# Performance work log

Hardware: AMD Instinct MI355X
Metric: run time of the kernel (lower is better)

## Reference

```python
import jax, jax.numpy as jnp
import numpy as np

N_EMBD = 768
N_HEAD = 12
HEAD_SIZE = N_EMBD // N_HEAD  # 64
WINDOW = 64  # sliding_window_size
EPS = 1e-6


def _rmsnorm(x, g):
    xf = x.astype(jnp.float32)
    n = xf * jax.lax.rsqrt(jnp.mean(xf * xf, axis=-1, keepdims=True) + EPS)
    return n.astype(x.dtype) * g


def _gelu_tanh(x):
    c = jnp.sqrt(jnp.asarray(2.0 / jnp.pi, x.dtype))
    return 0.5 * x * (1.0 + jnp.tanh(c * (x + 0.044715 * x ** 3)))


def setup_inputs() -> dict:
    key = jax.random.key(0)
    ks = jax.random.split(key, 12)
    B, T = 8, 1024
    s = 0.02
    return {
        "x": jax.random.normal(ks[0], (B, T, N_EMBD), jnp.float32),
        "w_q": jax.random.normal(ks[1], (N_EMBD, N_HEAD, HEAD_SIZE), jnp.float32) * s,
        "w_k": jax.random.normal(ks[2], (N_EMBD, N_HEAD, HEAD_SIZE), jnp.float32) * s,
        "w_v": jax.random.normal(ks[3], (N_EMBD, N_HEAD, HEAD_SIZE), jnp.float32) * s,
        "w_proj": jax.random.normal(ks[4], (N_EMBD, N_EMBD), jnp.float32) * s,
        "b_proj": jnp.zeros((N_EMBD,), jnp.float32),
        "w_ff1": jax.random.normal(ks[5], (N_EMBD, 4 * N_EMBD), jnp.float32) * s,
        "b_ff1": jnp.zeros((4 * N_EMBD,), jnp.float32),
        "w_ff2": jax.random.normal(ks[6], (4 * N_EMBD, N_EMBD), jnp.float32) * s,
        "b_ff2": jnp.zeros((N_EMBD,), jnp.float32),
        "g1": jnp.ones((N_EMBD,), jnp.float32),
        "g2": jnp.ones((N_EMBD,), jnp.float32),
    }


def reference(x, w_q, w_k, w_v, w_proj, b_proj, w_ff1, b_ff1, w_ff2, b_ff2, g1, g2):
    B, T, C = x.shape
    # ---- multi-head sliding-window causal attention (eval: dropout = identity) ----
    h = _rmsnorm(x, g1)
    q = jnp.einsum("btc,chd->bhtd", h, w_q)
    k = jnp.einsum("btc,chd->bhtd", h, w_k)
    v = jnp.einsum("btc,chd->bhtd", h, w_v)
    scores = jnp.einsum("bhtd,bhsd->bhts", q, k) / jnp.sqrt(jnp.asarray(HEAD_SIZE, x.dtype))
    pos = jnp.arange(T)
    diff = pos[:, None] - pos[None, :]  # q_pos - k_pos
    mask = (diff < 0) | (diff >= WINDOW)  # causal + sliding window of 64
    scores = jnp.where(mask[None, None], jnp.asarray(-jnp.inf, scores.dtype), scores)
    attn = jax.nn.softmax(scores, axis=-1)
    out = jnp.einsum("bhts,bhsd->bhtd", attn, v)
    out = out.transpose(0, 2, 1, 3).reshape(B, T, C)  # concat heads
    x = x + out @ w_proj + b_proj
    # ---- feedforward ----
    h2 = _rmsnorm(x, g2)
    ff = _gelu_tanh(h2 @ w_ff1 + b_ff1) @ w_ff2 + b_ff2
    x = x + ff
    aux = jnp.asarray(0.0, jnp.float32)
    return (x, aux)
```

## Files before the change

kernel.cpp:

```cpp
#include <hip/hip_runtime.h>
#include <cstdint>

#define DEVI __device__ __forceinline__

typedef __bf16 bf16x8 __attribute__((ext_vector_type(8)));
typedef float  f32x4  __attribute__((ext_vector_type(4)));

template<int V> struct IC { static constexpr int v = V; };

DEVI unsigned short f2b(float f){
  unsigned u = __builtin_bit_cast(unsigned, f);
  unsigned r = u + 0x7FFF + ((u >> 16) & 1);
  return (unsigned short)(r >> 16);
}
DEVI float b2f(unsigned short s){
  unsigned u = ((unsigned)s) << 16;
  return __builtin_bit_cast(float, u);
}
DEVI float gelu_f(float x){
  float u = 0.7978845608028654f * (x + 0.044715f * x * x * x);
  float e = __expf(2.0f * u);
  return x * (1.0f - 1.0f / (e + 1.0f));
}
DEVI void gl_lds16(const unsigned short* g, unsigned short* l){
  __builtin_amdgcn_global_load_lds(
      (const __attribute__((address_space(1))) unsigned int*)g,
      (__attribute__((address_space(3))) unsigned int*)l, 16, 0, 0);
}

__global__ __launch_bounds__(256)
void transpose_all(const float* __restrict__ w_q, const float* __restrict__ w_k,
                   const float* __restrict__ w_v, const float* __restrict__ w_proj,
                   const float* __restrict__ w_ff1, const float* __restrict__ w_ff2,
                   unsigned short* __restrict__ WqkvT, unsigned short* __restrict__ WprojT,
                   unsigned short* __restrict__ Wff1T, unsigned short* __restrict__ Wff2T)
{
  __shared__ float tile[32][33];
  int blk = blockIdx.x;
  const float* in; unsigned short* out; int R, C, b0;
  if      (blk < 576) { in = w_q;    out = WqkvT;              R = 768;  C = 768;  b0 = 0;    }
  else if (blk < 1152){ in = w_k;    out = WqkvT + 768 * 768;  R = 768;  C = 768;  b0 = 576;  }
  else if (blk < 1728){ in = w_v;    out = WqkvT + 1536 * 768; R = 768;  C = 768;  b0 = 1152; }
  else if (blk < 2304){ in = w_proj; out = WprojT;             R = 768;  C = 768;  b0 = 1728; }
  else if (blk < 4608){ in = w_ff1;  out = Wff1T;              R = 768;  C = 3072; b0 = 2304; }
  else                { in = w_ff2;  out = Wff2T;              R = 3072; C = 768;  b0 = 4608; }
  int lb = blk - b0;
  int nbx = C >> 5;
  int bx = lb % nbx, by = lb / nbx;
  int c0 = bx << 5, r0 = by << 5;
  int tx = threadIdx.x & 31, ty = threadIdx.x >> 5;
  #pragma unroll
  for (int j = 0; j < 32; j += 8)
    tile[ty + j][tx] = in[(size_t)(r0 + ty + j) * C + c0 + tx];
  __syncthreads();
  #pragma unroll
  for (int j = 0; j < 32; j += 8)
    out[(size_t)(c0 + ty + j) * R + r0 + tx] = f2b(tile[tx][ty + j]);
}

template<bool INF32>
__global__ __launch_bounds__(256)
void rmsnorm_k(const void* __restrict__ xin, const float* __restrict__ g,
               unsigned short* __restrict__ out)
{
  int wid = threadIdx.x >> 6, lane = threadIdx.x & 63;
  size_t row = (size_t)blockIdx.x * 4 + wid;
  float v[12];
  float ss = 0.0f;
  if (INF32){
    const float* xr = (const float*)xin + row * 768;
    #pragma unroll
    for (int c = 0; c < 3; c++){
      float4 t = *(const float4*)&xr[lane * 4 + c * 256];
      v[c * 4 + 0] = t.x; v[c * 4 + 1] = t.y; v[c * 4 + 2] = t.z; v[c * 4 + 3] = t.w;
    }
  } else {
    const unsigned short* xr = (const unsigned short*)xin + row * 768;
    #pragma unroll
    for (int c = 0; c < 3; c++){
      ushort4 t = *(const ushort4*)&xr[lane * 4 + c * 256];
      v[c * 4 + 0] = b2f(t.x); v[c * 4 + 1] = b2f(t.y);
      v[c * 4 + 2] = b2f(t.z); v[c * 4 + 3] = b2f(t.w);
    }
  }
  #pragma unroll
  for (int j = 0; j < 12; j++) ss += v[j] * v[j];
  #pragma unroll
  for (int o = 32; o >= 1; o >>= 1) ss += __shfl_xor(ss, o);
  float rs = rsqrtf(ss * (1.0f / 768.0f) + 1e-6f);
  #pragma unroll
  for (int c = 0; c < 3; c++){
    const float4 gv = *(const float4*)&g[lane * 4 + c * 256];
    ushort4 o4;
    o4.x = f2b(v[c * 4 + 0] * rs * gv.x);
    o4.y = f2b(v[c * 4 + 1] * rs * gv.y);
    o4.z = f2b(v[c * 4 + 2] * rs * gv.z);
    o4.w = f2b(v[c * 4 + 3] * rs * gv.w);
    *(ushort4*)&out[row * 768 + lane * 4 + c * 256] = o4;
  }
}

template<int BM, int TPB, bool BIAS, bool GELU_, int RESM, bool OUTF32>
__global__ __launch_bounds__(256, BM == 64 ? 3 : 2)
void gemm_db(const unsigned short* __restrict__ A, const unsigned short* __restrict__ Bt,
             const float* __restrict__ bias, const void* __restrict__ res,
             void* __restrict__ outp, int M, int N, int K)
{
  constexpr int MI = BM / 32;
  constexpr int AL = BM / 32;
  constexpr int BUFSZ = (BM + 128) * 64;
  __shared__ unsigned short sm[2][BUFSZ];

  int tid = threadIdx.x, wid = tid >> 6, lane = tid & 63;
  int la = lane & 15, hi = lane >> 4;
  int wm = wid >> 1, wn = wid & 1;
  int tiles_n = N >> 7;
  int bid = blockIdx.x;
  bid = (bid & 7) * (gridDim.x >> 3) + (bid >> 3);
  int g0 = bid * TPB;
  int NT = K >> 6;

  size_t constA[AL]; unsigned short* aDst[2][AL];
  size_t constB[4];  unsigned short* bDst[2][4];
  #pragma unroll
  for (int l = 0; l < AL; l++){
    int cb = wid * (BM * 2) + l * 64;
    int idx = cb + lane;
    int row = idx >> 3, sl2 = (idx & 7) ^ (row & 7);
    constA[l] = (size_t)row * K + sl2 * 8;
    aDst[0][l] = &sm[0][cb * 8];
    aDst[1][l] = &sm[1][cb * 8];
  }
  #pragma unroll
  for (int l = 0; l < 4; l++){
    int cb = wid * 256 + l * 64;
    int idx = cb + lane;
    int row = idx >> 3, sl2 = (idx & 7) ^ (row & 7);
    constB[l] = (size_t)row * K + sl2 * 8;
    bDst[0][l] = &sm[0][BM * 64 + cb * 8];
    bDst[1][l] = &sm[1][BM * 64 + cb * 8];
  }

  const unsigned short* fa[2][2];
  const unsigned short* fb[2][2];
  #pragma unroll
  for (int bf = 0; bf < 2; bf++)
    #pragma unroll
    for (int kk = 0; kk < 2; kk++){
      int sw = (((kk * 4 + hi) ^ (la & 7))) * 8;
      fa[bf][kk] = &sm[bf][(wm * (BM / 2) + la) * 64 + sw];
      fb[bf][kk] = &sm[bf][BM * 64 + (wn * 64 + la) * 64 + sw];
    }

  const unsigned short* aSrc[AL];
  const unsigned short* bSrc[4];
  auto setSrc = [&](int g){
    int m0 = (g / tiles_n) * BM, n0 = (g % tiles_n) << 7;
    #pragma unroll
    for (int l = 0; l < AL; l++) aSrc[l] = A  + (size_t)m0 * K + constA[l];
    #pragma unroll
    for (int l = 0; l < 4;  l++) bSrc[l] = Bt + (size_t)n0 * K + constB[l];
  };
  auto stageTo = [&](auto BF){
    constexpr int bf = decltype(BF)::v;
    #pragma unroll
    for (int l = 0; l < AL; l++){ gl_lds16(aSrc[l], aDst[bf][l]); aSrc[l] += 64; }
    #pragma unroll
    for (int l = 0; l < 4; l++){ gl_lds16(bSrc[l], bDst[bf][l]); bSrc[l] += 64; }
  };

  setSrc(g0);
  stageTo(IC<0>{});

  float* outF = (float*)outp;
  unsigned short* outB = (unsigned short*)outp;
  const float* resF = (const float*)res;
  const unsigned short* resB = (const unsigned short*)res;

  for (int ot = 0; ot < TPB; ot++){
    int g = g0 + ot;
    int m0 = (g / tiles_n) * BM, n0 = (g % tiles_n) << 7;

    f32x4 acc[MI][4] = {};

    auto tile_step = [&](auto BUF, int t){
      constexpr int CB = decltype(BUF)::v;
      asm volatile("s_waitcnt vmcnt(0)" ::: "memory");
      __builtin_amdgcn_s_barrier();
      __builtin_amdgcn_sched_barrier(0);
      if (t + 1 < NT || ot + 1 < TPB){
        if (t + 1 == NT) setSrc(g + 1);
        stageTo(IC<CB ^ 1>{});
      }

      bf16x8 afr[MI][2], bfr[4][2];
      #pragma unroll
      for (int mm = 0; mm < MI; mm++){
        afr[mm][0] = *(const bf16x8*)(fa[CB][0] + mm * 1024);
        afr[mm][1] = *(const bf16x8*)(fa[CB][1] + mm * 1024);
      }
      #pragma unroll
      for (int nn = 0; nn < 4; nn++){
        bfr[nn][0] = *(const bf16x8*)(fb[CB][0] + nn * 1024);
        bfr[nn][1] = *(const bf16x8*)(fb[CB][1] + nn * 1024);
      }
      __builtin_amdgcn_s_setprio(1);
      #pragma unroll
      for (int mm = 0; mm < MI; mm++)
        #pragma unroll
        for (int nn = 0; nn < 4; nn++)
          #pragma unroll
          for (int kk = 0; kk < 2; kk++)
            acc[mm][nn] = __builtin_amdgcn_mfma_f32_16x16x32_bf16(
                afr[mm][kk], bfr[nn][kk], acc[mm][nn], 0, 0, 0);
      __builtin_amdgcn_s_setprio(0);
    };

    for (int t = 0; t < NT; t += 2){
      tile_step(IC<0>{}, t);
      tile_step(IC<1>{}, t + 1);
    }

    #pragma unroll
    for (int mm = 0; mm < MI; mm++){
      int rowb = m0 + wm * (BM / 2) + mm * 16 + hi * 4;
      #pragma unroll
      for (int nn = 0; nn < 4; nn++){
        int col = n0 + wn * 64 + nn * 16 + la;
        float bv = BIAS ? bias[col] : 0.0f;
        #pragma unroll
        for (int r = 0; r < 4; r++){
          float val = acc[mm][nn][r] + bv;
          if (GELU_) val = gelu_f(val);
          size_t o = (size_t)(rowb + r) * N + col;
          if (RESM == 1) val += resF[o];
          if (RESM == 2) val += b2f(resB[o]);
          if (OUTF32) outF[o] = val;
          else        outB[o] = f2b(val);
        }
      }
    }
  }
}

__global__ __launch_bounds__(256)
void attn_k(const unsigned short* __restrict__ qkv, unsigned short* __restrict__ attn)
{
  __shared__ unsigned short Qs[64 * 72];
  __shared__ unsigned short Ks[128 * 72];
  __shared__ unsigned short Vt[64 * 136];
  __shared__ unsigned short Ps[4][16 * 136];

  int tid = threadIdx.x, wid = tid >> 6, lane = tid & 63;
  int la = lane & 15, hi = lane >> 4;
  int blk = blockIdx.x;
  blk = (blk & 7) * (gridDim.x >> 3) + (blk >> 3);
  int tile = blk & 15, hb = blk >> 4;
  int h = hb % 12, b = hb / 12;
  int t0 = tile << 6;

  const unsigned short* qbase = qkv + (size_t)(b * 1024) * 2304 + h * 64;

  #pragma unroll
  for (int r = 0; r < 2; r++){
    int idx = tid + r * 256;
    int row = idx >> 3, ch = idx & 7;
    uint4 v = *(const uint4*)(qbase + (size_t)(t0 + row) * 2304 + ch * 8);
    *(uint4*)&Qs[row * 72 + ch * 8] = v;
  }
  #pragma unroll
  for (int r = 0; r < 4; r++){
    int idx = tid + r * 256;
    int row = idx >> 3, ch = idx & 7;
    int sg = t0 - 64 + row; sg = sg < 0 ? 0 : sg;
    uint4 v = *(const uint4*)(qbase + 768 + (size_t)sg * 2304 + ch * 8);
    *(uint4*)&Ks[row * 72 + ch * 8] = v;
  }
  #pragma unroll
  for (int r = 0; r < 4; r++){
    int idx = tid + r * 256;
    int s = idx & 127, ch = idx >> 7;
    int sg = t0 - 64 + s; sg = sg < 0 ? 0 : sg;
    uint4 v = *(const uint4*)(qbase + 1536 + (size_t)sg * 2304 + ch * 8);
    unsigned short tmp[8];
    *(uint4*)tmp = v;
    #pragma unroll
    for (int j = 0; j < 8; j++)
      Vt[(ch * 8 + j) * 136 + s] = tmp[j];
  }
  __syncthreads();

  f32x4 sc[8];
  #pragma unroll
  for (int sj = 0; sj < 8; sj++) sc[sj] = (f32x4){0.f, 0.f, 0.f, 0.f};
  #pragma unroll
  for (int kk = 0; kk < 2; kk++){
    bf16x8 aq = *(const bf16x8*)&Qs[(wid * 16 + la) * 72 + kk * 32 + hi * 8];
    #pragma unroll
    for (int sj = 0; sj < 8; sj++){
      bf16x8 bk = *(const bf16x8*)&Ks[(sj * 16 + la) * 72 + kk * 32 + hi * 8];
      sc[sj] = __builtin_amdgcn_mfma_f32_16x16x32_bf16(aq, bk, sc[sj], 0, 0, 0);
    }
  }

  float inv[4];
  #pragma unroll
  for (int r2 = 0; r2 < 4; r2++){
    int row = wid * 16 + hi * 4 + r2;
    float mx = -1e30f;
    #pragma unroll
    for (int sj = 0; sj < 8; sj++){
      int sl = sj * 16 + la;
      bool valid = (sl >= row + 1) && (sl <= row + 64) && (t0 - 64 + sl >= 0);
      float sv = valid ? sc[sj][r2] * 0.125f : -1e30f;
      sc[sj][r2] = sv;
      mx = fmaxf(mx, sv);
    }
    #pragma unroll
    for (int o = 8; o >= 1; o >>= 1) mx = fmaxf(mx, __shfl_xor(mx, o));
    float sum = 0.0f;
    #pragma unroll
    for (int sj = 0; sj < 8; sj++){
      float p = __expf(sc[sj][r2] - mx);
      sc[sj][r2] = p;
      sum += p;
    }
    #pragma unroll
    for (int o = 8; o >= 1; o >>= 1) sum += __shfl_xor(sum, o);
    inv[r2] = 1.0f / sum;
  }

  unsigned short* myP = Ps[wid];
  #pragma unroll
  for (int sj = 0; sj < 8; sj++)
    #pragma unroll
    for (int r2 = 0; r2 < 4; r2++)
      myP[(hi * 4 + r2) * 136 + sj * 16 + la] = f2b(sc[sj][r2]);

  __syncthreads();

  f32x4 oacc[4];
  #pragma unroll
  for (int nj = 0; nj < 4; nj++) oacc[nj] = (f32x4){0.f, 0.f, 0.f, 0.f};
  #pragma unroll
  for (int ks = 0; ks < 4; ks++){
    bf16x8 ap = *(const bf16x8*)&myP[la * 136 + ks * 32 + hi * 8];
    #pragma unroll
    for (int nj = 0; nj < 4; nj++){
      bf16x8 bv = *(const bf16x8*)&Vt[(nj * 16 + la) * 136 + ks * 32 + hi * 8];
      oacc[nj] = __builtin_amdgcn_mfma_f32_16x16x32_bf16(ap, bv, oacc[nj], 0, 0, 0);
    }
  }

  unsigned short* obase = attn + (size_t)(b * 1024 + t0) * 768 + h * 64;
  #pragma unroll
  for (int nj = 0; nj < 4; nj++)
    #pragma unroll
    for (int r2 = 0; r2 < 4; r2++){
      int row = wid * 16 + hi * 4 + r2;
      obase[(size_t)row * 768 + nj * 16 + la] = f2b(oacc[nj][r2] * inv[r2]);
    }
}

__global__ void aux_k(float* p){ if (threadIdx.x == 0) p[0] = 0.0f; }

extern "C" void kernel_launch(void* const* d_in, const int* in_sizes, int n_in,
                              void* d_out, int out_size, void* d_ws, size_t ws_size,
                              hipStream_t stream)
{
  const float* x      = (const float*)d_in[0];
  const float* w_q    = (const float*)d_in[1];
  const float* w_k    = (const float*)d_in[2];
  const float* w_v    = (const float*)d_in[3];
  const float* w_proj = (const float*)d_in[4];
  const float* b_proj = (const float*)d_in[5];
  const float* w_ff1  = (const float*)d_in[6];
  const float* b_ff1  = (const float*)d_in[7];
  const float* w_ff2  = (const float*)d_in[8];
  const float* b_ff2  = (const float*)d_in[9];
  const float* g1     = (const float*)d_in[10];
  const float* g2     = (const float*)d_in[11];
  float* out = (float*)d_out;

  char* ws = (char*)d_ws;
  size_t off = 0;
  auto alloc = [&](size_t bytes){ size_t r = off; off += (bytes + 255) & ~(size_t)255; return r; };
  const size_t BT = 8 * 1024;

  unsigned short* h     = (unsigned short*)(ws + alloc(BT * 768 * 2));
  unsigned short* qkv   = (unsigned short*)(ws + alloc(BT * 3072 * 2));
  unsigned short* x2b   = (unsigned short*)(ws + alloc(BT * 768 * 2));
  unsigned short* h2    = (unsigned short*)(ws + alloc(BT * 768 * 2));
  unsigned short* WqkvT = (unsigned short*)(ws + alloc(2304 * 768 * 2));
  unsigned short* WprojT= (unsigned short*)(ws + alloc(768 * 768 * 2));
  unsigned short* Wff1T = (unsigned short*)(ws + alloc(3072 * 768 * 2));
  unsigned short* Wff2T = (unsigned short*)(ws + alloc(768 * 3072 * 2));
  unsigned short* attn  = h;
  unsigned short* ffa   = qkv;

  transpose_all<<<6912, 256, 0, stream>>>(w_q, w_k, w_v, w_proj, w_ff1, w_ff2,
                                          WqkvT, WprojT, Wff1T, Wff2T);

  rmsnorm_k<true><<<2048, 256, 0, stream>>>(x, g1, h);

  gemm_db<64,3,false,false,0,false><<<768, 256, 0, stream>>>(h, WqkvT, nullptr, nullptr, qkv, 8192, 2304, 768);

  attn_k<<<8 * 12 * 16, 256, 0, stream>>>(qkv, attn);

  gemm_db<64,1,true,false,1,false><<<768, 256, 0, stream>>>(attn, WprojT, b_proj, x, x2b, 8192, 768, 768);

  rmsnorm_k<false><<<2048, 256, 0, stream>>>(x2b, g2, h2);

  gemm_db<128,3,true,true,0,false><<<512, 256, 0, stream>>>(h2, Wff1T, b_ff1, nullptr, ffa, 8192, 3072, 768);

  gemm_db<64,1,true,false,2,true><<<768, 256, 0, stream>>>(ffa, Wff2T, b_ff2, x2b, out, 8192, 768, 3072);

  aux_k<<<1, 64, 0, stream>>>(out + 6291456);
}
```

Baseline: 200.9 us.

## Replace double-buffered GEMM with triple-buffered K=32 pipeline and register prefetch

```diff
diff --git a/kernel.cpp b/kernel.cpp
--- a/kernel.cpp
+++ b/kernel.cpp
@@ -100,16 +100,14 @@
   }
 }
 
-template<int BM, int TPB, bool BIAS, bool GELU_, int RESM, bool OUTF32>
-__global__ __launch_bounds__(256, BM == 64 ? 3 : 2)
-void gemm_db(const unsigned short* __restrict__ A, const unsigned short* __restrict__ Bt,
+template<int TPB, bool BIAS, bool GELU_, int RESM, bool OUTF32>
+__global__ __launch_bounds__(256, 4)
+void gemm_pl(const unsigned short* __restrict__ A, const unsigned short* __restrict__ Bt,
              const float* __restrict__ bias, const void* __restrict__ res,
              void* __restrict__ outp, int M, int N, int K)
 {
-  constexpr int MI = BM / 32;
-  constexpr int AL = BM / 32;
-  constexpr int BUFSZ = (BM + 128) * 64;
-  __shared__ unsigned short sm[2][BUFSZ];
+  constexpr int BUFS = (64 + 128) * 32;
+  __shared__ unsigned short sm[3][BUFS];
 
   int tid = threadIdx.x, wid = tid >> 6, lane = tid & 63;
   int la = lane & 15, hi = lane >> 4;
@@ -118,59 +116,73 @@
   int bid = blockIdx.x;
   bid = (bid & 7) * (gridDim.x >> 3) + (bid >> 3);
   int g0 = bid * TPB;
-  int NT = K >> 6;
-
-  size_t constA[AL]; unsigned short* aDst[2][AL];
-  size_t constB[4];  unsigned short* bDst[2][4];
-  #pragma unroll
-  for (int l = 0; l < AL; l++){
-    int cb = wid * (BM * 2) + l * 64;
-    int idx = cb + lane;
-    int row = idx >> 3, sl2 = (idx & 7) ^ (row & 7);
-    constA[l] = (size_t)row * K + sl2 * 8;
-    aDst[0][l] = &sm[0][cb * 8];
-    aDst[1][l] = &sm[1][cb * 8];
-  }
-  #pragma unroll
-  for (int l = 0; l < 4; l++){
-    int cb = wid * 256 + l * 64;
-    int idx = cb + lane;
-    int row = idx >> 3, sl2 = (idx & 7) ^ (row & 7);
+  int NT = K >> 5;
+  int TOT = NT * TPB;
+
+  size_t constA;  size_t constB[2];
+  {
+    int idx = wid * 64 + lane;
+    int row = idx >> 2, sl2 = (idx & 3) ^ ((row >> 1) & 3);
+    constA = (size_t)row * K + sl2 * 8;
+  }
+  #pragma unroll
+  for (int l = 0; l < 2; l++){
+    int idx = wid * 128 + l * 64 + lane;
+    int row = idx >> 2, sl2 = (idx & 3) ^ ((row >> 1) & 3);
     constB[l] = (size_t)row * K + sl2 * 8;
-    bDst[0][l] = &sm[0][BM * 64 + cb * 8];
-    bDst[1][l] = &sm[1][BM * 64 + cb * 8];
-  }
-
-  const unsigned short* fa[2][2];
-  const unsigned short* fb[2][2];
-  #pragma unroll
-  for (int bf = 0; bf < 2; bf++)
-    #pragma unroll
-    for (int kk = 0; kk < 2; kk++){
-      int sw = (((kk * 4 + hi) ^ (la & 7))) * 8;
-      fa[bf][kk] = &sm[bf][(wm * (BM / 2) + la) * 64 + sw];
-      fb[bf][kk] = &sm[bf][BM * 64 + (wn * 64 + la) * 64 + sw];
-    }
-
-  const unsigned short* aSrc[AL];
-  const unsigned short* bSrc[4];
+  }
+  unsigned short* aDst[3];
+  unsigned short* bDst[3][2];
+  #pragma unroll
+  for (int b = 0; b < 3; b++){
+    aDst[b] = &sm[b][(wid * 64) * 8];
+    bDst[b][0] = &sm[b][2048 + (wid * 128) * 8];
+    bDst[b][1] = &sm[b][2048 + (wid * 128 + 64) * 8];
+  }
+
+  const unsigned short* fa[3];
+  const unsigned short* fb[3];
+  {
+    int sw = (hi ^ ((la >> 1) & 3)) * 8;
+    #pragma unroll
+    for (int b = 0; b < 3; b++){
+      fa[b] = &sm[b][(wm * 32 + la) * 32 + sw];
+      fb[b] = &sm[b][2048 + (wn * 64 + la) * 32 + sw];
+    }
+  }
+
+  const unsigned short* aSrc;
+  const unsigned short* bSrc[2];
   auto setSrc = [&](int g){
-    int m0 = (g / tiles_n) * BM, n0 = (g % tiles_n) << 7;
-    #pragma unroll
-    for (int l = 0; l < AL; l++) aSrc[l] = A  + (size_t)m0 * K + constA[l];
-    #pragma unroll
-    for (int l = 0; l < 4;  l++) bSrc[l] = Bt + (size_t)n0 * K + constB[l];
+    int m0 = (g / tiles_n) * 64, n0 = (g % tiles_n) << 7;
+    aSrc = A + (size_t)m0 * K + constA;
+    bSrc[0] = Bt + (size_t)n0 * K + constB[0];
+    bSrc[1] = Bt + (size_t)n0 * K + constB[1];
   };
   auto stageTo = [&](auto BF){
-    constexpr int bf = decltype(BF)::v;
-    #pragma unroll
-    for (int l = 0; l < AL; l++){ gl_lds16(aSrc[l], aDst[bf][l]); aSrc[l] += 64; }
-    #pragma unroll
-    for (int l = 0; l < 4; l++){ gl_lds16(bSrc[l], bDst[bf][l]); bSrc[l] += 64; }
+    constexpr int b = decltype(BF)::v;
+    gl_lds16(aSrc, aDst[b]);            aSrc += 32;
+    gl_lds16(bSrc[0], bDst[b][0]);      bSrc[0] += 32;
+    gl_lds16(bSrc[1], bDst[b][1]);      bSrc[1] += 32;
+  };
+
+  bf16x8 frA[2][2], frB[2][4];
+  auto readTo = [&](auto BF, auto RG){
+    constexpr int b = decltype(BF)::v, r = decltype(RG)::v;
+    frA[r][0] = *(const bf16x8*)(fa[b]);
+    frA[r][1] = *(const bf16x8*)(fa[b] + 512);
+    frB[r][0] = *(const bf16x8*)(fb[b]);
+    frB[r][1] = *(const bf16x8*)(fb[b] + 512);
+    frB[r][2] = *(const bf16x8*)(fb[b] + 1024);
+    frB[r][3] = *(const bf16x8*)(fb[b] + 1536);
   };
 
   setSrc(g0);
   stageTo(IC<0>{});
+  stageTo(IC<1>{});
+  asm volatile("s_waitcnt vmcnt(3)" ::: "memory");
+  __builtin_amdgcn_s_barrier();
+  readTo(IC<0>{}, IC<0>{});
 
   float* outF = (float*)outp;
   unsigned short* outB = (unsigned short*)outp;
@@ -179,51 +191,44 @@
 
   for (int ot = 0; ot < TPB; ot++){
     int g = g0 + ot;
-    int m0 = (g / tiles_n) * BM, n0 = (g % tiles_n) << 7;
-
-    f32x4 acc[MI][4] = {};
-
-    auto tile_step = [&](auto BUF, int t){
-      constexpr int CB = decltype(BUF)::v;
+    int m0 = (g / tiles_n) * 64, n0 = (g % tiles_n) << 7;
+    f32x4 acc[2][4] = {};
+
+    auto body = [&](auto BUFc, auto REGc, int t){
+      constexpr int cb = decltype(BUFc)::v;
+      constexpr int cr = decltype(REGc)::v;
       asm volatile("s_waitcnt vmcnt(0)" ::: "memory");
       __builtin_amdgcn_s_barrier();
       __builtin_amdgcn_sched_barrier(0);
-      if (t + 1 < NT || ot + 1 < TPB){
-        if (t + 1 == NT) setSrc(g + 1);
-        stageTo(IC<CB ^ 1>{});
+      int s = ot * NT + t;
+      if (s + 2 < TOT){
+        if (t + 2 == NT) setSrc(g + 1);
+        stageTo(IC<(cb + 2) % 3>{});
       }
-
-      bf16x8 afr[MI][2], bfr[4][2];
-      #pragma unroll
-      for (int mm = 0; mm < MI; mm++){
-        afr[mm][0] = *(const bf16x8*)(fa[CB][0] + mm * 1024);
-        afr[mm][1] = *(const bf16x8*)(fa[CB][1] + mm * 1024);
-      }
-      #pragma unroll
-      for (int nn = 0; nn < 4; nn++){
-        bfr[nn][0] = *(const bf16x8*)(fb[CB][0] + nn * 1024);
-        bfr[nn][1] = *(const bf16x8*)(fb[CB][1] + nn * 1024);
-      }
+      if (s + 1 < TOT)
+        readTo(IC<(cb + 1) % 3>{}, IC<(cr + 1) % 2>{});
       __builtin_amdgcn_s_setprio(1);
       #pragma unroll
-      for (int mm = 0; mm < MI; mm++)
+      for (int mm = 0; mm < 2; mm++)
         #pragma unroll
         for (int nn = 0; nn < 4; nn++)
-          #pragma unroll
-          for (int kk = 0; kk < 2; kk++)
-            acc[mm][nn] = __builtin_amdgcn_mfma_f32_16x16x32_bf16(
-                afr[mm][kk], bfr[nn][kk], acc[mm][nn], 0, 0, 0);
+          acc[mm][nn] = __builtin_amdgcn_mfma_f32_16x16x32_bf16(
+              frA[cr][mm], frB[cr][nn], acc[mm][nn], 0, 0, 0);
       __builtin_amdgcn_s_setprio(0);
     };
 
-    for (int t = 0; t < NT; t += 2){
-      tile_step(IC<0>{}, t);
-      tile_step(IC<1>{}, t + 1);
-    }
-
-    #pragma unroll
-    for (int mm = 0; mm < MI; mm++){
-      int rowb = m0 + wm * (BM / 2) + mm * 16 + hi * 4;
+    for (int t = 0; t < NT; t += 6){
+      body(IC<0>{}, IC<0>{}, t + 0);
+      body(IC<1>{}, IC<1>{}, t + 1);
+      body(IC<2>{}, IC<0>{}, t + 2);
+      body(IC<0>{}, IC<1>{}, t + 3);
+      body(IC<1>{}, IC<0>{}, t + 4);
+      body(IC<2>{}, IC<1>{}, t + 5);
+    }
+
+    #pragma unroll
+    for (int mm = 0; mm < 2; mm++){
+      int rowb = m0 + wm * 32 + mm * 16 + hi * 4;
       #pragma unroll
       for (int nn = 0; nn < 4; nn++){
         int col = n0 + wn * 64 + nn * 16 + la;
@@ -403,17 +408,17 @@
 
   rmsnorm_k<true><<<2048, 256, 0, stream>>>(x, g1, h);
 
-  gemm_db<64,3,false,false,0,false><<<768, 256, 0, stream>>>(h, WqkvT, nullptr, nullptr, qkv, 8192, 2304, 768);
+  gemm_pl<3,false,false,0,false><<<768, 256, 0, stream>>>(h, WqkvT, nullptr, nullptr, qkv, 8192, 2304, 768);
 
   attn_k<<<8 * 12 * 16, 256, 0, stream>>>(qkv, attn);
 
-  gemm_db<64,1,true,false,1,false><<<768, 256, 0, stream>>>(attn, WprojT, b_proj, x, x2b, 8192, 768, 768);
+  gemm_pl<1,true,false,1,false><<<768, 256, 0, stream>>>(attn, WprojT, b_proj, x, x2b, 8192, 768, 768);
 
   rmsnorm_k<false><<<2048, 256, 0, stream>>>(x2b, g2, h2);
 
-  gemm_db<128,3,true,true,0,false><<<512, 256, 0, stream>>>(h2, Wff1T, b_ff1, nullptr, ffa, 8192, 3072, 768);
-
-  gemm_db<64,1,true,false,2,true><<<768, 256, 0, stream>>>(ffa, Wff2T, b_ff2, x2b, out, 8192, 768, 3072);
+  gemm_pl<3,true,true,0,false><<<1024, 256, 0, stream>>>(h2, Wff1T, b_ff1, nullptr, ffa, 8192, 3072, 768);
+
+  gemm_pl<1,true,false,2,true><<<768, 256, 0, stream>>>(ffa, Wff2T, b_ff2, x2b, out, 8192, 768, 3072);
 
   aux_k<<<1, 64, 0, stream>>>(out + 6291456);
 }
```

Measured after the change: 248.6 us. 1.24x slower.
